# Performance work log

Measured on AMD Instinct MI355X. Metric: run time of the kernel, lower is better.

## Reference

```python
import jax, jax.numpy as jnp
import numpy as np

B, S, HID, NH = 2, 2048, 1024, 16
HD = HID // NH
NEG = -1e10


def setup_inputs() -> dict:
    key = jax.random.key(0)
    ks = jax.random.split(key, 14)
    s = 0.02
    return {
        "query": jax.random.normal(ks[0], (B, S, HID), jnp.float32),
        "key_": jax.random.normal(ks[1], (B, S, HID), jnp.float32),
        "value": jax.random.normal(ks[2], (B, S, HID), jnp.float32),
        "mask": jax.random.randint(ks[3], (B, 1, 1, S), 0, 2, jnp.int32),
        "Wq": jax.random.normal(ks[4], (HID, HID), jnp.float32) * s,
        "bq": jnp.zeros((HID,), jnp.float32),
        "Wk": jax.random.normal(ks[5], (HID, HID), jnp.float32) * s,
        "bk": jnp.zeros((HID,), jnp.float32),
        "Wv": jax.random.normal(ks[6], (HID, HID), jnp.float32) * s,
        "bv": jnp.zeros((HID,), jnp.float32),
        "Ww": jax.random.normal(ks[7], (HD, HD), jnp.float32) * s,
        "bw": jnp.zeros((HD,), jnp.float32),
        "Wo": jax.random.normal(ks[8], (HID, HID), jnp.float32) * s,
        "bo": jnp.zeros((HID,), jnp.float32),
    }


def reference(query, key_, value, mask, Wq, bq, Wk, bk, Wv, bv, Ww, bw, Wo, bo):
    def heads(x, W, b):
        h = x @ W.T + b                       # [B,S,HID]
        return h.reshape(B, S, NH, HD).transpose(0, 2, 1, 3)  # [B,H,S,D]

    Q = heads(query, Wq, bq)
    K = heads(key_, Wk, bk)
    V = heads(value, Wv, bv)
    # multiplicative: per-head linear on Q before QK^T (no 1/sqrt(d) scale)
    Qw = Q @ Ww.T + bw                        # [B,H,S,D]
    energy = jnp.einsum('bhqd,bhkd->bhqk', Qw, K)
    energy = jnp.where(mask == 0, jnp.float32(NEG), energy)
    attention = jax.nn.softmax(energy, axis=-1)
    x = jnp.einsum('bhqk,bhkd->bhqd', attention, V)  # dropout p=0 (eval)
    x = x.transpose(0, 2, 1, 3).reshape(B, S, HID)
    x = x @ Wo.T + bo
    return (x, attention)
```

## Files before the change

kernel.cpp:

```cpp
#include <hip/hip_runtime.h>
#include <hip/hip_bf16.h>

#define B_    2
#define S_    2048
#define HID_  1024
#define NH_   16
#define HD_   64
#define M_    (B_ * S_)
#define NEGB_ (-1.0e30f)
#define LOG2E 1.44269504088896340736f
#define X_ELEMS 4194304

typedef __bf16 bf16;
typedef bf16  bf16x2 __attribute__((ext_vector_type(2)));
typedef bf16  bf16x4 __attribute__((ext_vector_type(4)));
typedef bf16  bf16x8 __attribute__((ext_vector_type(8)));
typedef float f32x4  __attribute__((ext_vector_type(4)));

static __device__ __forceinline__ f32x4 mfma16(bf16x8 a, bf16x8 b, f32x4 c) {
    return __builtin_amdgcn_mfma_f32_16x16x32_bf16(a, b, c, 0, 0, 0);
}

static __device__ __forceinline__ int pack2(float x, float y) {
    union { bf16x2 h; int i; } u;
    u.h = bf16x2{(bf16)x, (bf16)y};
    return u.i;
}

static __device__ __forceinline__ void barrier_lds() {
    asm volatile("s_waitcnt lgkmcnt(0)" ::: "memory");
    __builtin_amdgcn_s_barrier();
}

static __device__ __forceinline__ int swadr(int row, int chunk) {
    return row * 128 + ((chunk ^ (row & 7)) << 4);
}
static __device__ __forceinline__ bf16x8 lds8(const bf16* base, int row, int chunk) {
    return *(const bf16x8*)((const char*)base + swadr(row, chunk));
}


__global__ void cast3(const float* __restrict__ a, const float* __restrict__ b,
                      const float* __restrict__ c, bf16* __restrict__ oa,
                      bf16* __restrict__ ob, bf16* __restrict__ oc) {
    const float* in = blockIdx.y == 0 ? a : blockIdx.y == 1 ? b : c;
    bf16* out = blockIdx.y == 0 ? oa : blockIdx.y == 1 ? ob : oc;
    int i = (blockIdx.x * 256 + threadIdx.x) * 4;
    float4 v = *(const float4*)(in + i);
    out[i + 0] = (bf16)v.x;
    out[i + 1] = (bf16)v.y;
    out[i + 2] = (bf16)v.z;
    out[i + 3] = (bf16)v.w;
}

__global__ __launch_bounds__(256) void fuse_wq(const float* __restrict__ Ww,
                                               const float* __restrict__ Wq,
                                               const float* __restrict__ bq,
                                               const float* __restrict__ bw,
                                               bf16* __restrict__ Wq_eff,
                                               float* __restrict__ bq_eff) {
    __shared__ float ww[64][64];
    const int h = blockIdx.x >> 2, chunk = blockIdx.x & 3;
    const int i = chunk * 256 + threadIdx.x;
    for (int t = threadIdx.x; t < 4096; t += 256) ww[t >> 6][t & 63] = Ww[t];
    __syncthreads();
    float col[64];
    #pragma unroll
    for (int d = 0; d < 64; ++d) col[d] = Wq[(size_t)(h * 64 + d) * 1024 + i];
    for (int j = 0; j < 64; ++j) {
        float acc = 0.f;
        #pragma unroll
        for (int d = 0; d < 64; ++d) acc += ww[j][d] * col[d];
        Wq_eff[(size_t)(h * 64 + j) * 1024 + i] = (bf16)(acc * LOG2E);
    }
    if (chunk == 0 && threadIdx.x < 64) {
        int j = threadIdx.x;
        float acc = bw[j];
        for (int d = 0; d < 64; ++d) acc += ww[j][d] * bq[h * 64 + d];
        bq_eff[h * 64 + j] = acc * LOG2E;
    }
}

__global__ __launch_bounds__(256, 2) void proj3(const float* __restrict__ Aq,
                                                const float* __restrict__ Ak,
                                                const float* __restrict__ Av,
                                                const bf16* __restrict__ W0,
                                                const bf16* __restrict__ W1,
                                                const bf16* __restrict__ W2,
                                                const float* __restrict__ b0,
                                                const float* __restrict__ b1,
                                                const float* __restrict__ b2,
                                                bf16* __restrict__ Qw,
                                                bf16* __restrict__ Kh,
                                                bf16* __restrict__ Vt) {
    __shared__ __align__(16) bf16 Ast[2][128 * 64];
    __shared__ __align__(16) bf16 Wst[2][128 * 64];
    const int z = blockIdx.z;
    const float* A = z == 0 ? Aq : z == 1 ? Ak : Av;
    const bf16* W = z == 0 ? W0 : z == 1 ? W1 : W2;
    const float* bias = z == 0 ? b0 : z == 1 ? b1 : b2;

    const int tid = threadIdx.x;
    const int wave = tid >> 6, lane = tid & 63;
    const int lr = lane & 15, kg = lane >> 4;
    const int mb0 = blockIdx.x * 128;
    const int n0 = blockIdx.y * 128;

    const int arow = tid >> 1, akc = (tid & 1) * 32;
    const int wrow = tid >> 1, wkc = (tid & 1) * 32;

    float4 ar[8];
    bf16x8 wr[4];
    auto loadT = [&](int k0) {
        const float4* ap = (const float4*)(A + (size_t)(mb0 + arow) * HID_ + k0 + akc);
        #pragma unroll
        for (int j = 0; j < 8; ++j) ar[j] = ap[j];
        const bf16* wp = W + (size_t)(n0 + wrow) * HID_ + k0 + wkc;
        #pragma unroll
        for (int j = 0; j < 4; ++j) wr[j] = *(const bf16x8*)(wp + j * 8);
    };
    auto writeT = [&](int buf) {
        #pragma unroll
        for (int c = 0; c < 4; ++c) {
            float4 x0 = ar[2 * c], x1 = ar[2 * c + 1];
            bf16x8 v;
            v[0] = (bf16)x0.x; v[1] = (bf16)x0.y; v[2] = (bf16)x0.z; v[3] = (bf16)x0.w;
            v[4] = (bf16)x1.x; v[5] = (bf16)x1.y; v[6] = (bf16)x1.z; v[7] = (bf16)x1.w;
            *(bf16x8*)((char*)Ast[buf] + swadr(arow, (akc >> 3) + c)) = v;
        }
        #pragma unroll
        for (int c = 0; c < 4; ++c)
            *(bf16x8*)((char*)Wst[buf] + swadr(wrow, (wkc >> 3) + c)) = wr[c];
    };

    f32x4 acc[2][8] = {};
    loadT(0);
    for (int t = 0; t < 16; ++t) {
        const int buf = t & 1;
        writeT(buf);
        if (t < 15) loadT((t + 1) * 64);
        barrier_lds();
        const bf16* ab = Ast[buf];
        const bf16* wb = Wst[buf];
        #pragma unroll
        for (int kp = 0; kp < 2; ++kp) {
            bf16x8 af0 = lds8(ab, wave * 16 + lr, kp * 4 + kg);
            bf16x8 af1 = lds8(ab, 64 + wave * 16 + lr, kp * 4 + kg);
            #pragma unroll
            for (int nf = 0; nf < 8; ++nf) {
                bf16x8 wf = lds8(wb, nf * 16 + lr, kp * 4 + kg);
                acc[0][nf] = mfma16(af0, wf, acc[0][nf]);
                acc[1][nf] = mfma16(af1, wf, acc[1][nf]);
            }
        }
        barrier_lds();
    }

    const int m_base = mb0 + wave * 16;
    #pragma unroll
    for (int t = 0; t < 2; ++t) {
        #pragma unroll
        for (int cg = 0; cg < 8; ++cg) {
            int col = n0 + cg * 16 + lr;
            float bv = bias[col];
            int h = col >> 6, d = col & 63;
            #pragma unroll
            for (int r = 0; r < 4; ++r) {
                int m = m_base + t * 64 + kg * 4 + r;
                int b = m >> 11, s = m & 2047;
                float val = acc[t][cg][r] + bv;
                if (z == 0)
                    Qw[((size_t)(b * NH_ + h) * S_ + s) * HD_ + d] = (bf16)val;
                else if (z == 1)
                    Kh[((size_t)(b * NH_ + h) * S_ + s) * HD_ + d] = (bf16)val;
                else
                    Vt[((size_t)(b * NH_ + h) * HD_ + d) * S_ + s] = (bf16)val;
            }
        }
    }
}

__global__ __launch_bounds__(512, 4) void attn_sums(const bf16* __restrict__ Qw,
                                                    const bf16* __restrict__ Kh,
                                                    const int* __restrict__ mask,
                                                    float* __restrict__ lsum_g) {
    __shared__ __align__(16) float negf[S_];
    __shared__ __align__(16) bf16 Kst[2][4096];

    const int tid = threadIdx.x;
    const int lane = tid & 63, wave = tid >> 6;
    const int lr = lane & 15, kg = lane >> 4;

    const int wg = blockIdx.x;
    const int flat = (wg & 7) * 64 + (wg >> 3);
    const int qtile = flat & 15;
    const int bh = flat >> 4;
    const int b = bh >> 4;
    const int q0 = qtile * 128 + wave * 16;

    const bf16* Qh = Qw + (size_t)bh * S_ * HD_;
    const bf16* Kb = Kh + (size_t)bh * S_ * HD_;
    const int*  mb = mask + b * S_;

    for (int t = tid; t < S_; t += 512)
        negf[t] = mb[t] ? 0.f : NEGB_;

    const int srow = tid >> 3;
    const int sch  = tid & 7;
    const int sdst = swadr(srow, sch);

    bf16x8 a0 = *(const bf16x8*)(Qh + (size_t)(q0 + lr) * HD_ + kg * 8);
    bf16x8 a1 = *(const bf16x8*)(Qh + (size_t)(q0 + lr) * HD_ + 32 + kg * 8);

    __syncthreads();

    bf16x8 kreg = *(const bf16x8*)(Kb + (size_t)srow * HD_ + sch * 8);

    float psum = 0.f;
    for (int t = 0; t < 32; ++t) {
        const int buf = t & 1;
        *(bf16x8*)((char*)Kst[buf] + sdst) = kreg;
        if (t + 1 < 32)
            kreg = *(const bf16x8*)(Kb + (size_t)((t + 1) * 64 + srow) * HD_ + sch * 8);
        barrier_lds();
        const bf16* kb = Kst[buf];
        #pragma unroll
        for (int s2 = 0; s2 < 2; ++s2) {
            const int rlo = s2 * 32 + lr, rhi = s2 * 32 + 16 + lr;
            bf16x8 k0a = lds8(kb, rlo, kg);
            bf16x8 k1a = lds8(kb, rlo, 4 + kg);
            bf16x8 k0b = lds8(kb, rhi, kg);
            bf16x8 k1b = lds8(kb, rhi, 4 + kg);
            f32x4 e0 = *(const f32x4*)&negf[t * 64 + s2 * 32 + kg * 4];
            f32x4 e1 = *(const f32x4*)&negf[t * 64 + s2 * 32 + 16 + kg * 4];
            e0 = mfma16(k0a, a0, e0);
            e0 = mfma16(k1a, a1, e0);
            e1 = mfma16(k0b, a0, e1);
            e1 = mfma16(k1b, a1, e1);
            #pragma unroll
            for (int r = 0; r < 4; ++r)
                psum += exp2f(e0[r]) + exp2f(e1[r]);
        }
        barrier_lds();
    }

    psum += __shfl_xor(psum, 16);
    psum += __shfl_xor(psum, 32);
    if (lane < 16) lsum_g[(size_t)bh * S_ + q0 + lr] = psum;
}

__global__ __launch_bounds__(512, 4) void attn_main(const bf16* __restrict__ Qw,
                                                    const bf16* __restrict__ Kh,
                                                    const bf16* __restrict__ Vt,
                                                    const int* __restrict__ mask,
                                                    const float* __restrict__ lsum_g,
                                                    float* __restrict__ attn_out,
                                                    bf16* __restrict__ Xh) {
    __shared__ __align__(16) float negf[S_];
    __shared__ __align__(16) bf16 Kst[2][4096];
    __shared__ __align__(16) bf16 Vst[2][4096];

    const int tid = threadIdx.x;
    const int lane = tid & 63, wave = tid >> 6;
    const int lr = lane & 15, kg = lane >> 4;

    const int wg = blockIdx.x;
    const int flat = (wg & 7) * 64 + (wg >> 3);
    const int qtile = flat & 15;
    const int bh = flat >> 4;
    const int b = bh >> 4, h = bh & 15;
    const int q0 = qtile * 128 + wave * 16;

    const bf16* Qh = Qw + (size_t)bh * S_ * HD_;
    const bf16* Kb = Kh + (size_t)bh * S_ * HD_;
    const bf16* Vb = Vt + (size_t)bh * HD_ * S_;
    const int*  mb = mask + b * S_;
    float* arow = attn_out + (size_t)bh * S_ * S_;

    for (int t = tid; t < S_; t += 512)
        negf[t] = mb[t] ? 0.f : NEGB_;

    const int srow = tid >> 3;
    const int sch  = tid & 7;
    const int sdst = swadr(srow, sch);

    bf16x8 a0 = *(const bf16x8*)(Qh + (size_t)(q0 + lr) * HD_ + kg * 8);
    bf16x8 a1 = *(const bf16x8*)(Qh + (size_t)(q0 + lr) * HD_ + 32 + kg * 8);
    const float lg2l = __log2f(lsum_g[(size_t)bh * S_ + q0 + lr]);

    const int addrA = (lr + (((kg << 1)    ) & 3) * 16) << 2;
    const int addrB = (lr + (((kg << 1) | 1) & 3) * 16) << 2;
    const bool lt2 = kg < 2;

    __syncthreads();

    bf16x8 kreg = *(const bf16x8*)(Kb + (size_t)srow * HD_ + sch * 8);
    bf16x8 vreg = *(const bf16x8*)(Vb + (size_t)srow * S_ + sch * 8);

    f32x4 X[4] = {};
    for (int t = 0; t < 32; ++t) {
        const int buf = t & 1;
        *(bf16x8*)((char*)Kst[buf] + sdst) = kreg;
        *(bf16x8*)((char*)Vst[buf] + sdst) = vreg;
        if (t + 1 < 32) {
            kreg = *(const bf16x8*)(Kb + (size_t)((t + 1) * 64 + srow) * HD_ + sch * 8);
            vreg = *(const bf16x8*)(Vb + (size_t)srow * S_ + (t + 1) * 64 + sch * 8);
        }
        barrier_lds();
        const bf16* kb = Kst[buf];
        const bf16* vb = Vst[buf];
        #pragma unroll
        for (int s2 = 0; s2 < 2; ++s2) {
            const int rlo = s2 * 32 + lr, rhi = s2 * 32 + 16 + lr;
            bf16x8 k0a = lds8(kb, rlo, kg);
            bf16x8 k1a = lds8(kb, rlo, 4 + kg);
            bf16x8 k0b = lds8(kb, rhi, kg);
            bf16x8 k1b = lds8(kb, rhi, 4 + kg);
            f32x4 nb0 = *(const f32x4*)&negf[t * 64 + s2 * 32 + kg * 4];
            f32x4 nb1 = *(const f32x4*)&negf[t * 64 + s2 * 32 + 16 + kg * 4];
            f32x4 e0, e1;
            #pragma unroll
            for (int r = 0; r < 4; ++r) { e0[r] = nb0[r] - lg2l; e1[r] = nb1[r] - lg2l; }
            e0 = mfma16(k0a, a0, e0);
            e0 = mfma16(k1a, a1, e0);
            e1 = mfma16(k0b, a0, e1);
            e1 = mfma16(k1b, a1, e1);
            f32x4 p0, p1;
            #pragma unroll
            for (int r = 0; r < 4; ++r) { p0[r] = exp2f(e0[r]); p1[r] = exp2f(e1[r]); }
            *(f32x4*)(arow + (size_t)(q0 + lr) * S_ + t * 64 + s2 * 32 + kg * 4) = p0;
            *(f32x4*)(arow + (size_t)(q0 + lr) * S_ + t * 64 + s2 * 32 + 16 + kg * 4) = p1;
            int q0d = pack2(p0[0], p0[1]);
            int q1d = pack2(p0[2], p0[3]);
            int q2d = pack2(p1[0], p1[1]);
            int q3d = pack2(p1[2], p1[3]);
            int bA0 = __builtin_amdgcn_ds_bpermute(addrA, q0d);
            int bA1 = __builtin_amdgcn_ds_bpermute(addrA, q1d);
            int bA2 = __builtin_amdgcn_ds_bpermute(addrA, q2d);
            int bA3 = __builtin_amdgcn_ds_bpermute(addrA, q3d);
            int bB0 = __builtin_amdgcn_ds_bpermute(addrB, q0d);
            int bB1 = __builtin_amdgcn_ds_bpermute(addrB, q1d);
            int bB2 = __builtin_amdgcn_ds_bpermute(addrB, q2d);
            int bB3 = __builtin_amdgcn_ds_bpermute(addrB, q3d);
            union { int d[4]; bf16x8 v; } pau;
            pau.d[0] = lt2 ? bA0 : bA2;
            pau.d[1] = lt2 ? bA1 : bA3;
            pau.d[2] = lt2 ? bB0 : bB2;
            pau.d[3] = lt2 ? bB1 : bB3;
            #pragma unroll
            for (int ds = 0; ds < 4; ++ds) {
                bf16x8 v = lds8(vb, ds * 16 + lr, s2 * 4 + kg);
                X[ds] = mfma16(v, pau.v, X[ds]);
            }
        }
        barrier_lds();
    }

    bf16* xrow = Xh + ((size_t)(b * S_ + q0 + lr)) * HID_ + h * HD_;
    #pragma unroll
    for (int ds = 0; ds < 4; ++ds) {
        bf16x4 xv;
        #pragma unroll
        for (int r = 0; r < 4; ++r) xv[r] = (bf16)X[ds][r];
        *(bf16x4*)(xrow + ds * 16 + kg * 4) = xv;
    }
}

__global__ __launch_bounds__(256, 3) void out_gemm(const bf16* __restrict__ X,
                                                   const bf16* __restrict__ Wo,
                                                   const float* __restrict__ bo,
                                                   float* __restrict__ out) {
    __shared__ __align__(16) bf16 Ast[2][128 * 64];
    __shared__ __align__(16) bf16 Wst[2][64 * 64];

    const int tid = threadIdx.x;
    const int wave = tid >> 6, lane = tid & 63;
    const int lr = lane & 15, kg = lane >> 4;
    const int mb0 = blockIdx.x * 128;
    const int n0 = blockIdx.y * 64;

    const int arow = tid >> 1, akc = (tid & 1) * 32;
    const int wrow = tid >> 2, wkc = (tid & 3) * 16;

    bf16x8 ar[4];
    bf16x8 wr[2];
    auto loadT = [&](int k0) {
        const bf16* ap = X + (size_t)(mb0 + arow) * HID_ + k0 + akc;
        #pragma unroll
        for (int j = 0; j < 4; ++j) ar[j] = *(const bf16x8*)(ap + j * 8);
        const bf16* wp = Wo + (size_t)(n0 + wrow) * HID_ + k0 + wkc;
        wr[0] = *(const bf16x8*)wp;
        wr[1] = *(const bf16x8*)(wp + 8);
    };
    auto writeT = [&](int buf) {
        #pragma unroll
        for (int c = 0; c < 4; ++c)
            *(bf16x8*)((char*)Ast[buf] + swadr(arow, (akc >> 3) + c)) = ar[c];
        *(bf16x8*)((char*)Wst[buf] + swadr(wrow, wkc >> 3)) = wr[0];
        *(bf16x8*)((char*)Wst[buf] + swadr(wrow, (wkc >> 3) + 1)) = wr[1];
    };

    f32x4 acc[2][4] = {};
    loadT(0);
    for (int t = 0; t < 16; ++t) {
        const int buf = t & 1;
        writeT(buf);
        if (t < 15) loadT((t + 1) * 64);
        barrier_lds();
        const bf16* ab = Ast[buf];
        const bf16* wb = Wst[buf];
        #pragma unroll
        for (int kp = 0; kp < 2; ++kp) {
            bf16x8 af0 = lds8(ab, wave * 16 + lr, kp * 4 + kg);
            bf16x8 af1 = lds8(ab, 64 + wave * 16 + lr, kp * 4 + kg);
            #pragma unroll
            for (int nf = 0; nf < 4; ++nf) {
                bf16x8 wf = lds8(wb, nf * 16 + lr, kp * 4 + kg);
                acc[0][nf] = mfma16(af0, wf, acc[0][nf]);
                acc[1][nf] = mfma16(af1, wf, acc[1][nf]);
            }
        }
        barrier_lds();
    }

    const int m_base = mb0 + wave * 16;
    #pragma unroll
    for (int t = 0; t < 2; ++t) {
        #pragma unroll
        for (int cg = 0; cg < 4; ++cg) {
            int col = n0 + cg * 16 + lr;
            float bv = bo[col];
            #pragma unroll
            for (int r = 0; r < 4; ++r)
                out[(size_t)(m_base + t * 64 + kg * 4 + r) * HID_ + col] = acc[t][cg][r] + bv;
        }
    }
}

extern "C" void kernel_launch(void* const* d_in, const int* in_sizes, int n_in,
                              void* d_out, int out_size, void* d_ws, size_t ws_size,
                              hipStream_t stream) {
    const float* query = (const float*)d_in[0];
    const float* key_  = (const float*)d_in[1];
    const float* value = (const float*)d_in[2];
    const int*   mask  = (const int*)d_in[3];
    const float* Wq = (const float*)d_in[4];
    const float* bq = (const float*)d_in[5];
    const float* Wk = (const float*)d_in[6];
    const float* bk = (const float*)d_in[7];
    const float* Wv = (const float*)d_in[8];
    const float* bv = (const float*)d_in[9];
    const float* Ww = (const float*)d_in[10];
    const float* bw = (const float*)d_in[11];
    const float* Wo = (const float*)d_in[12];
    const float* bo = (const float*)d_in[13];
    float* out = (float*)d_out;

    char* ws = (char*)d_ws;
    size_t off = 0;
    auto alloc = [&](size_t bytes) {
        void* p = ws + off;
        off += (bytes + 255) & ~(size_t)255;
        return p;
    };
    bf16*  Wq_eff = (bf16*)alloc((size_t)HID_ * HID_ * 2);
    float* bq_eff = (float*)alloc((size_t)HID_ * 4);
    bf16*  Wk_b   = (bf16*)alloc((size_t)HID_ * HID_ * 2);
    bf16*  Wv_b   = (bf16*)alloc((size_t)HID_ * HID_ * 2);
    bf16*  Wo_b   = (bf16*)alloc((size_t)HID_ * HID_ * 2);
    bf16*  Qw     = (bf16*)alloc((size_t)M_ * HID_ * 2);
    bf16*  Kh     = (bf16*)alloc((size_t)M_ * HID_ * 2);
    bf16*  Vt     = (bf16*)alloc((size_t)M_ * HID_ * 2);
    bf16*  Xh     = (bf16*)alloc((size_t)M_ * HID_ * 2);
    float* lsum_g = (float*)alloc((size_t)B_ * NH_ * S_ * 4);
    (void)ws_size; (void)in_sizes; (void)n_in; (void)out_size;

    dim3 gcast(1024, 3);
    cast3<<<gcast, 256, 0, stream>>>(Wk, Wv, Wo, Wk_b, Wv_b, Wo_b);
    fuse_wq<<<64, 256, 0, stream>>>(Ww, Wq, bq, bw, Wq_eff, bq_eff);

    dim3 gproj(M_ / 128, HID_ / 128, 3);
    proj3<<<gproj, 256, 0, stream>>>(query, key_, value,
                                     Wq_eff, Wk_b, Wv_b,
                                     bq_eff, bk, bv,
                                     Qw, Kh, Vt);

    attn_sums<<<512, 512, 0, stream>>>(Qw, Kh, mask, lsum_g);
    attn_main<<<512, 512, 0, stream>>>(Qw, Kh, Vt, mask, lsum_g, out + X_ELEMS, Xh);

    dim3 gout(M_ / 128, HID_ / 64);
    out_gemm<<<gout, 256, 0, stream>>>(Xh, Wo_b, bo, out);
}
```

Measured before the change: 330.1 us.

## Split attention key dimension in halves across workgroups with partial-sum merge

Both attention kernels now split the key/value sequence into two halves handled by separate workgroups, doubling the grid to 1024 blocks and halving each block's loop length. Row sums are stored per half and added in attn_main, and partial P·V outputs are written in fp32 to a scratch buffer. A new merge_x kernel adds the halves and converts to bf16 for the output GEMM. The aim is more parallelism and occupancy (launch bounds raised), at the cost of an extra kernel launch and extra fp32 partial traffic.

```diff
diff --git a/kernel.cpp b/kernel.cpp
--- a/kernel.cpp
+++ b/kernel.cpp
@@ -10,6 +10,7 @@
 #define NEGB_ (-1.0e30f)
 #define LOG2E 1.44269504088896340736f
 #define X_ELEMS 4194304
+#define BH_   (B_ * NH_)
 
 typedef __bf16 bf16;
 typedef bf16  bf16x2 __attribute__((ext_vector_type(2)));
@@ -180,11 +181,11 @@
     }
 }
 
-__global__ __launch_bounds__(512, 4) void attn_sums(const bf16* __restrict__ Qw,
+__global__ __launch_bounds__(512, 8) void attn_sums(const bf16* __restrict__ Qw,
                                                     const bf16* __restrict__ Kh,
                                                     const int* __restrict__ mask,
                                                     float* __restrict__ lsum_g) {
-    __shared__ __align__(16) float negf[S_];
+    __shared__ __align__(16) float negf[S_ / 2];
     __shared__ __align__(16) bf16 Kst[2][4096];
 
     const int tid = threadIdx.x;
@@ -192,17 +193,19 @@
     const int lr = lane & 15, kg = lane >> 4;
 
     const int wg = blockIdx.x;
-    const int flat = (wg & 7) * 64 + (wg >> 3);
-    const int qtile = flat & 15;
-    const int bh = flat >> 4;
+    const int flat = (wg & 7) * 128 + (wg >> 3);
+    const int half = flat & 1;
+    const int qtile = (flat >> 1) & 15;
+    const int bh = flat >> 5;
     const int b = bh >> 4;
     const int q0 = qtile * 128 + wave * 16;
+    const int kv0 = half * (S_ / 2);
 
     const bf16* Qh = Qw + (size_t)bh * S_ * HD_;
     const bf16* Kb = Kh + (size_t)bh * S_ * HD_;
-    const int*  mb = mask + b * S_;
-
-    for (int t = tid; t < S_; t += 512)
+    const int*  mb = mask + b * S_ + kv0;
+
+    for (int t = tid; t < S_ / 2; t += 512)
         negf[t] = mb[t] ? 0.f : NEGB_;
 
     const int srow = tid >> 3;
@@ -214,14 +217,14 @@
 
     __syncthreads();
 
-    bf16x8 kreg = *(const bf16x8*)(Kb + (size_t)srow * HD_ + sch * 8);
+    bf16x8 kreg = *(const bf16x8*)(Kb + (size_t)(kv0 + srow) * HD_ + sch * 8);
 
     float psum = 0.f;
-    for (int t = 0; t < 32; ++t) {
+    for (int t = 0; t < 16; ++t) {
         const int buf = t & 1;
         *(bf16x8*)((char*)Kst[buf] + sdst) = kreg;
-        if (t + 1 < 32)
-            kreg = *(const bf16x8*)(Kb + (size_t)((t + 1) * 64 + srow) * HD_ + sch * 8);
+        if (t + 1 < 16)
+            kreg = *(const bf16x8*)(Kb + (size_t)(kv0 + (t + 1) * 64 + srow) * HD_ + sch * 8);
         barrier_lds();
         const bf16* kb = Kst[buf];
         #pragma unroll
@@ -246,17 +249,18 @@
 
     psum += __shfl_xor(psum, 16);
     psum += __shfl_xor(psum, 32);
-    if (lane < 16) lsum_g[(size_t)bh * S_ + q0 + lr] = psum;
-}
-
-__global__ __launch_bounds__(512, 4) void attn_main(const bf16* __restrict__ Qw,
+    if (lane < 16)
+        lsum_g[(size_t)half * (BH_ * S_) + (size_t)bh * S_ + q0 + lr] = psum;
+}
+
+__global__ __launch_bounds__(512, 6) void attn_main(const bf16* __restrict__ Qw,
                                                     const bf16* __restrict__ Kh,
                                                     const bf16* __restrict__ Vt,
                                                     const int* __restrict__ mask,
                                                     const float* __restrict__ lsum_g,
                                                     float* __restrict__ attn_out,
-                                                    bf16* __restrict__ Xh) {
-    __shared__ __align__(16) float negf[S_];
+                                                    float* __restrict__ Xp) {
+    __shared__ __align__(16) float negf[S_ / 2];
     __shared__ __align__(16) bf16 Kst[2][4096];
     __shared__ __align__(16) bf16 Vst[2][4096];
 
@@ -265,19 +269,21 @@
     const int lr = lane & 15, kg = lane >> 4;
 
     const int wg = blockIdx.x;
-    const int flat = (wg & 7) * 64 + (wg >> 3);
-    const int qtile = flat & 15;
-    const int bh = flat >> 4;
-    const int b = bh >> 4, h = bh & 15;
+    const int flat = (wg & 7) * 128 + (wg >> 3);
+    const int half = flat & 1;
+    const int qtile = (flat >> 1) & 15;
+    const int bh = flat >> 5;
+    const int b = bh >> 4;
     const int q0 = qtile * 128 + wave * 16;
+    const int kv0 = half * (S_ / 2);
 
     const bf16* Qh = Qw + (size_t)bh * S_ * HD_;
     const bf16* Kb = Kh + (size_t)bh * S_ * HD_;
     const bf16* Vb = Vt + (size_t)bh * HD_ * S_;
-    const int*  mb = mask + b * S_;
-    float* arow = attn_out + (size_t)bh * S_ * S_;
-
-    for (int t = tid; t < S_; t += 512)
+    const int*  mb = mask + b * S_ + kv0;
+    float* arow = attn_out + (size_t)bh * S_ * S_ + kv0;
+
+    for (int t = tid; t < S_ / 2; t += 512)
         negf[t] = mb[t] ? 0.f : NEGB_;
 
     const int srow = tid >> 3;
@@ -286,7 +292,8 @@
 
     bf16x8 a0 = *(const bf16x8*)(Qh + (size_t)(q0 + lr) * HD_ + kg * 8);
     bf16x8 a1 = *(const bf16x8*)(Qh + (size_t)(q0 + lr) * HD_ + 32 + kg * 8);
-    const float lg2l = __log2f(lsum_g[(size_t)bh * S_ + q0 + lr]);
+    const size_t lidx = (size_t)bh * S_ + q0 + lr;
+    const float lg2l = __log2f(lsum_g[lidx] + lsum_g[(size_t)BH_ * S_ + lidx]);
 
     const int addrA = (lr + (((kg << 1)    ) & 3) * 16) << 2;
     const int addrB = (lr + (((kg << 1) | 1) & 3) * 16) << 2;
@@ -294,17 +301,17 @@
 
     __syncthreads();
 
-    bf16x8 kreg = *(const bf16x8*)(Kb + (size_t)srow * HD_ + sch * 8);
-    bf16x8 vreg = *(const bf16x8*)(Vb + (size_t)srow * S_ + sch * 8);
+    bf16x8 kreg = *(const bf16x8*)(Kb + (size_t)(kv0 + srow) * HD_ + sch * 8);
+    bf16x8 vreg = *(const bf16x8*)(Vb + (size_t)srow * S_ + kv0 + sch * 8);
 
     f32x4 X[4] = {};
-    for (int t = 0; t < 32; ++t) {
+    for (int t = 0; t < 16; ++t) {
         const int buf = t & 1;
         *(bf16x8*)((char*)Kst[buf] + sdst) = kreg;
         *(bf16x8*)((char*)Vst[buf] + sdst) = vreg;
-        if (t + 1 < 32) {
-            kreg = *(const bf16x8*)(Kb + (size_t)((t + 1) * 64 + srow) * HD_ + sch * 8);
-            vreg = *(const bf16x8*)(Vb + (size_t)srow * S_ + (t + 1) * 64 + sch * 8);
+        if (t + 1 < 16) {
+            kreg = *(const bf16x8*)(Kb + (size_t)(kv0 + (t + 1) * 64 + srow) * HD_ + sch * 8);
+            vreg = *(const bf16x8*)(Vb + (size_t)srow * S_ + kv0 + (t + 1) * 64 + sch * 8);
         }
         barrier_lds();
         const bf16* kb = Kst[buf];
@@ -356,14 +363,32 @@
         barrier_lds();
     }
 
-    bf16* xrow = Xh + ((size_t)(b * S_ + q0 + lr)) * HID_ + h * HD_;
+    float* xrow = Xp + ((size_t)half * BH_ + bh) * S_ * 64 + (size_t)(q0 + lr) * 64;
     #pragma unroll
-    for (int ds = 0; ds < 4; ++ds) {
-        bf16x4 xv;
-        #pragma unroll
-        for (int r = 0; r < 4; ++r) xv[r] = (bf16)X[ds][r];
-        *(bf16x4*)(xrow + ds * 16 + kg * 4) = xv;
-    }
+    for (int ds = 0; ds < 4; ++ds)
+        *(f32x4*)(xrow + ds * 16 + kg * 4) = X[ds];
+}
+
+__global__ __launch_bounds__(256) void merge_x(const float* __restrict__ Xp,
+                                               bf16* __restrict__ Xh) {
+    const int g = blockIdx.x * 256 + threadIdx.x;
+    const int d0 = (g & 7) * 8;
+    const int hs = g >> 3;
+    const int h = hs & 15;
+    const int m = hs >> 4;
+    const int b = m >> 11, s = m & 2047;
+    const size_t pbase = ((size_t)(b * NH_ + h)) * S_ * 64 + (size_t)s * 64 + d0;
+    f32x4 x0a = *(const f32x4*)(Xp + pbase);
+    f32x4 x0b = *(const f32x4*)(Xp + pbase + 4);
+    f32x4 x1a = *(const f32x4*)(Xp + (size_t)BH_ * S_ * 64 + pbase);
+    f32x4 x1b = *(const f32x4*)(Xp + (size_t)BH_ * S_ * 64 + pbase + 4);
+    bf16x8 o;
+    #pragma unroll
+    for (int r = 0; r < 4; ++r) {
+        o[r]     = (bf16)(x0a[r] + x1a[r]);
+        o[4 + r] = (bf16)(x0b[r] + x1b[r]);
+    }
+    *(bf16x8*)(Xh + (size_t)m * HID_ + h * 64 + d0) = o;
 }
 
 __global__ __launch_bounds__(256, 3) void out_gemm(const bf16* __restrict__ X,
@@ -472,7 +497,8 @@
     bf16*  Kh     = (bf16*)alloc((size_t)M_ * HID_ * 2);
     bf16*  Vt     = (bf16*)alloc((size_t)M_ * HID_ * 2);
     bf16*  Xh     = (bf16*)alloc((size_t)M_ * HID_ * 2);
-    float* lsum_g = (float*)alloc((size_t)B_ * NH_ * S_ * 4);
+    float* lsum_g = (float*)alloc((size_t)2 * BH_ * S_ * 4);
+    float* Xp     = (float*)alloc((size_t)2 * BH_ * S_ * 64 * 4);
     (void)ws_size; (void)in_sizes; (void)n_in; (void)out_size;
 
     dim3 gcast(1024, 3);
@@ -485,8 +511,9 @@
                                      bq_eff, bk, bv,
                                      Qw, Kh, Vt);
 
-    attn_sums<<<512, 512, 0, stream>>>(Qw, Kh, mask, lsum_g);
-    attn_main<<<512, 512, 0, stream>>>(Qw, Kh, Vt, mask, lsum_g, out + X_ELEMS, Xh);
+    attn_sums<<<1024, 512, 0, stream>>>(Qw, Kh, mask, lsum_g);
+    attn_main<<<1024, 512, 0, stream>>>(Qw, Kh, Vt, mask, lsum_g, out + X_ELEMS, Xp);
+    merge_x<<<2048, 256, 0, stream>>>(Xp, Xh);
 
     dim3 gout(M_ / 128, HID_ / 64);
     out_gemm<<<gout, 256, 0, stream>>>(Xh, Wo_b, bo, out);
```

Measured after the change: 343.2 us. 1.04x slower.
